# Optimization experiments

Measured on AMD Instinct MI355X. Metric: run time of the kernel, lower is better.

Reference implementation:

```python
import jax, jax.numpy as jnp
import numpy as np
from jax import lax

L, E, H, V, B, S = 25, 64, 8, 30000, 1000, 512


def setup_inputs() -> dict:
    key = jax.random.key(0)
    ks = jax.random.split(key, 24)
    p = lambda k, shape: (jax.random.normal(k, shape) * 0.1).astype(jnp.float32)
    inp = {
        "x": jax.random.randint(ks[0], (B, S), 0, V),
        "embedding": p(ks[1], (V, E)),
        # layer 0 (input dim = E)
        "W_xz0": p(ks[2], (E, H)), "W_hz0": p(ks[3], (H, H)), "b_z0": p(ks[4], (H,)),
        "W_xr0": p(ks[5], (E, H)), "W_hr0": p(ks[6], (H, H)), "b_r0": p(ks[7], (H,)),
        "W_xH0": p(ks[8], (E, H)), "W_rH0": p(ks[9], (H, H)), "b_H0": p(ks[10], (H,)),
        # layers 1..L-1 stacked (input dim = H)
        "W_xz": p(ks[11], (L - 1, H, H)), "W_hz": p(ks[12], (L - 1, H, H)), "b_z": p(ks[13], (L - 1, H)),
        "W_xr": p(ks[14], (L - 1, H, H)), "W_hr": p(ks[15], (L - 1, H, H)), "b_r": p(ks[16], (L - 1, H)),
        "W_xH": p(ks[17], (L - 1, H, H)), "W_rH": p(ks[18], (L - 1, H, H)), "b_H": p(ks[19], (L - 1, H)),
        "W_hy": p(ks[20], (H, 1)), "b_y": p(ks[21], (1,)),
    }
    return inp


def _cell(x_t, h, Wxz, Whz, bz, Wxr, Whr, br, WxH, WrH, bH):
    z = jax.nn.sigmoid(x_t @ Wxz + h @ Whz + bz)
    r = jax.nn.sigmoid(x_t @ Wxr + h @ Whr + br)
    Hc = jnp.tanh(x_t @ WxH + (h * r) @ WrH + bH)
    return h * (1.0 - z) + z * Hc


def reference(x, embedding, W_xz0, W_hz0, b_z0, W_xr0, W_hr0, b_r0, W_xH0, W_rH0, b_H0,
              W_xz, W_hz, b_z, W_xr, W_hr, b_r, W_xH, W_rH, b_H, W_hy, b_y):
    emb = embedding[x]                     # [B, S, E]
    bsz = x.shape[0]
    h0 = jnp.zeros((L, bsz, H), dtype=embedding.dtype)

    def time_step(h_all, x_t):            # h_all: [L, B, H]; x_t: [B, E]
        h_new0 = _cell(x_t, h_all[0], W_xz0, W_hz0, b_z0, W_xr0, W_hr0, b_r0, W_xH0, W_rH0, b_H0)

        def layer_step(inp_t, ws):
            Wxz, Whz, bz, Wxr, Whr, br, WxH, WrH, bH, h_prev = ws
            h_new = _cell(inp_t, h_prev, Wxz, Whz, bz, Wxr, Whr, br, WxH, WrH, bH)
            return h_new, h_new

        _, h_rest = lax.scan(layer_step, h_new0,
                             (W_xz, W_hz, b_z, W_xr, W_hr, b_r, W_xH, W_rH, b_H, h_all[1:]))
        return jnp.concatenate([h_new0[None], h_rest], axis=0), None

    h_last, _ = lax.scan(time_step, h0, jnp.swapaxes(emb, 0, 1))  # scan over S
    logits = h_last[-1] @ W_hy + b_y       # [B, 1]
    return logits.squeeze(-1), h_last
```

## Files before the change

### kernel.cpp

```cpp
#include <hip/hip_runtime.h>
#include <hip/hip_bf16.h>
#include <stdint.h>

#define L_ 25
#define E_ 64
#define H_ 8
#define B_ 1000
#define S_ 512
#define GQ 4
#define NCELL (L_ * GQ)
#define TPBR (NCELL * 8)
#define TS 4
#define NSUPER (S_ / TS + L_ - 1)
#define HS 12
#define XG 36

typedef float v2f __attribute__((ext_vector_type(2)));
typedef float v4f __attribute__((ext_vector_type(4)));

#define PIN(x) asm volatile("" : "+v"(x))

__device__ __forceinline__ v2f pkfma(v2f a, v2f b, v2f c) {
  v2f d;
  asm("v_pk_fma_f32 %0, %1, %2, %3" : "=v"(d) : "v"(a), "v"(b), "v"(c));
  return d;
}
__device__ __forceinline__ v2f pkfma_l(v2f a, v2f b, v2f c) {
  v2f d;
  asm("v_pk_fma_f32 %0, %1, %2, %3 op_sel:[0,0,0] op_sel_hi:[0,1,1]"
      : "=v"(d) : "v"(a), "v"(b), "v"(c));
  return d;
}
__device__ __forceinline__ v2f pkfma_h(v2f a, v2f b, v2f c) {
  v2f d;
  asm("v_pk_fma_f32 %0, %1, %2, %3 op_sel:[1,0,0] op_sel_hi:[1,1,1]"
      : "=v"(d) : "v"(a), "v"(b), "v"(c));
  return d;
}
__device__ __forceinline__ v2f pkadd(v2f a, v2f b) {
  v2f d;
  asm("v_pk_add_f32 %0, %1, %2" : "=v"(d) : "v"(a), "v"(b));
  return d;
}
__device__ __forceinline__ v2f vlo(v4f v) { return __builtin_shufflevector(v, v, 0, 1); }
__device__ __forceinline__ v2f vhi(v4f v) { return __builtin_shufflevector(v, v, 2, 3); }
__device__ __forceinline__ v2f mk2(float a, float b) { v2f r; r.x = a; r.y = b; return r; }

#define CHAIN8(acc, ma, mb, w)            \
  acc = pkfma_l(vlo(ma), w[0], acc);      \
  acc = pkfma_h(vlo(ma), w[1], acc);      \
  acc = pkfma_l(vhi(ma), w[2], acc);      \
  acc = pkfma_h(vhi(ma), w[3], acc);      \
  acc = pkfma_l(vlo(mb), w[4], acc);      \
  acc = pkfma_h(vlo(mb), w[5], acc);      \
  acc = pkfma_l(vhi(mb), w[6], acc);      \
  acc = pkfma_h(vhi(mb), w[7], acc);

#define CHAIN4P(acc, ma, mb, w)           \
  acc = pkfma(vlo(ma), w[0], acc);        \
  acc = pkfma(vhi(ma), w[1], acc);        \
  acc = pkfma(vlo(mb), w[2], acc);        \
  acc = pkfma(vhi(mb), w[3], acc);

__device__ __forceinline__ float ulo(uint32_t u) { return __uint_as_float(u << 16); }
__device__ __forceinline__ float uhi(uint32_t u) { return __uint_as_float(u & 0xffff0000u); }

__device__ __forceinline__ float toF(float v) { return v; }
__device__ __forceinline__ float toF(__hip_bfloat16 v) { return __bfloat162float(v); }
__device__ __forceinline__ void stP(float* p, float v) { *p = v; }
__device__ __forceinline__ void stP(__hip_bfloat16* p, float v) { *p = __float2bfloat16(v); }

__device__ __forceinline__ v2f loadC2(const float* p) { return *(const v2f*)p; }
__device__ __forceinline__ v2f loadC2(const __hip_bfloat16* p) {
  const uint32_t u = *(const uint32_t*)p;
  return mk2(ulo(u), uhi(u));
}

__device__ __forceinline__ void load8f(const __hip_bfloat16* p, float* o) {
  const uint4 v = *(const uint4*)p;
  o[0] = ulo(v.x); o[1] = uhi(v.x); o[2] = ulo(v.y); o[3] = uhi(v.y);
  o[4] = ulo(v.z); o[5] = uhi(v.z); o[6] = ulo(v.w); o[7] = uhi(v.w);
}
__device__ __forceinline__ void load8f(const float* p, float* o) {
  const float4 a = ((const float4*)p)[0];
  const float4 b = ((const float4*)p)[1];
  o[0] = a.x; o[1] = a.y; o[2] = a.z; o[3] = a.w;
  o[4] = b.x; o[5] = b.y; o[6] = b.z; o[7] = b.w;
}

__device__ __forceinline__ void st4(float* p, float a, float b, float c, float d) {
  float4 v; v.x = a; v.y = b; v.z = c; v.w = d;
  *(float4*)p = v;
}
__device__ __forceinline__ void st4(__hip_bfloat16* p, float a, float b, float c, float d) {
  __hip_bfloat16 t[4] = {__float2bfloat16(a), __float2bfloat16(b),
                         __float2bfloat16(c), __float2bfloat16(d)};
  *(ushort4*)p = *(ushort4*)t;
}

__device__ __forceinline__ float sigmo(float x) {
  return __builtin_amdgcn_rcpf(1.f + __expf(-x));
}

__device__ __forceinline__ void detect64(const unsigned short* __restrict__ u,
                                         int tid, float* fl) {
  if (tid < 64) {
    float m = 0.f;
#pragma unroll
    for (int k = 0; k < 4; ++k) {
      const uint32_t q = u[tid * 4 + k];
      float v = fabsf(__uint_as_float(q << 16));
      if (!(v < 1e30f)) v = 1e30f;
      m = fmaxf(m, v);
    }
#pragma unroll
    for (int off = 32; off; off >>= 1) m = fmaxf(m, __shfl_down(m, off, 64));
    if (tid == 0) *fl = (m > 2.0f) ? 0.f : 1.f;
  }
}

template <typename T, typename PT>
__device__ __forceinline__ void pre_body(
    const int* __restrict__ x, const void* __restrict__ embv,
    const void* __restrict__ Wzv, const void* __restrict__ Wrv,
    const void* __restrict__ Whv, PT* __restrict__ pre,
    float* WL, float* TBb) {
  const T* emb = (const T*)embv;
  const T* Wz = (const T*)Wzv;
  const T* Wr = (const T*)Wrv;
  const T* Wh = (const T*)Whv;
  const int tid = threadIdx.x;

  for (int idx = tid; idx < 64 * 24; idx += 256) {
    const int k = idx / 24, c = idx - k * 24;
    float w;
    if (c < 16) w = toF(((c & 1) ? Wr : Wz)[k * 8 + (c >> 1)]);
    else        w = toF(Wh[k * 8 + (c - 16)]);
    WL[idx] = w;
  }
  __syncthreads();

  const int tok = blockIdx.x * 256 + tid;
  const int t = x[tok];

  v2f acc[12];
#pragma unroll
  for (int q = 0; q < 12; ++q) acc[q] = mk2(0.f, 0.f);

  for (int kb = 0; kb < 8; ++kb) {
    float e[8];
    load8f(emb + (size_t)t * E_ + kb * 8, e);
#pragma unroll
    for (int k8 = 0; k8 < 8; ++k8) {
      const v4f* wr = (const v4f*)(WL + (kb * 8 + k8) * 24);
      const v2f ee = mk2(e[k8], e[k8]);
#pragma unroll
      for (int q = 0; q < 6; ++q) {
        const v4f w4 = wr[q];
        acc[2 * q]     = pkfma(ee, vlo(w4), acc[2 * q]);
        acc[2 * q + 1] = pkfma(ee, vhi(w4), acc[2 * q + 1]);
      }
    }
  }

  const int wid = tid >> 6, lane = tid & 63;
  float* tb = TBb + wid * (24 * 65);
#pragma unroll
  for (int q = 0; q < 12; ++q) {
    tb[(2 * q) * 65 + lane] = acc[q].x;
    tb[(2 * q + 1) * 65 + lane] = acc[q].y;
  }
  asm volatile("s_waitcnt lgkmcnt(0)" ::: "memory");
  __builtin_amdgcn_wave_barrier();

  PT* ob = pre + (size_t)(blockIdx.x * 256 + wid * 64) * 24;
#pragma unroll
  for (int it = 0; it < 6; ++it) {
    const int F0 = it * 256 + lane * 4;
    float o[4];
#pragma unroll
    for (int e2 = 0; e2 < 4; ++e2) {
      const int F = F0 + e2;
      const int tk = F / 24;
      const int c = F - tk * 24;
      o[e2] = tb[c * 65 + tk];
    }
    st4(ob + F0, o[0], o[1], o[2], o[3]);
  }
}

template <typename PT>
__global__ __launch_bounds__(256, 4) void gru_pre(
    const int* __restrict__ x, const void* __restrict__ emb,
    const void* __restrict__ Wz, const void* __restrict__ Wr,
    const void* __restrict__ Wh, PT* __restrict__ pre) {
  __shared__ __align__(16) float WL[64 * 24];
  __shared__ __align__(16) float TB[4][24 * 65];
  __shared__ float fl;
  detect64((const unsigned short*)emb, threadIdx.x, &fl);
  __syncthreads();
  if (fl != 0.f) pre_body<__hip_bfloat16, PT>(x, emb, Wz, Wr, Wh, pre, WL, &TB[0][0]);
  else           pre_body<float, PT>(x, emb, Wz, Wr, Wh, pre, WL, &TB[0][0]);
}

template <typename T, typename PT>
__device__ __forceinline__ void rec_body(
    const PT* __restrict__ pre,
    const void* __restrict__ Whz0v, const void* __restrict__ bz0v,
    const void* __restrict__ Whr0v, const void* __restrict__ br0v,
    const void* __restrict__ WrH0v, const void* __restrict__ bH0v,
    const void* __restrict__ Wxzv, const void* __restrict__ Whzv,
    const void* __restrict__ bzv, const void* __restrict__ Wxrv,
    const void* __restrict__ Whrv, const void* __restrict__ brv,
    const void* __restrict__ WxHv, const void* __restrict__ WrHv,
    const void* __restrict__ bHv, const void* __restrict__ Whyv,
    const void* __restrict__ byv, void* __restrict__ outv,
    float* hrsh, float* xbuf) {
  const T* Whz0 = (const T*)Whz0v; const T* bz0 = (const T*)bz0v;
  const T* Whr0 = (const T*)Whr0v; const T* br0 = (const T*)br0v;
  const T* WrH0 = (const T*)WrH0v; const T* bH0 = (const T*)bH0v;
  const T* Wxz = (const T*)Wxzv;   const T* Whz = (const T*)Whzv;
  const T* bz = (const T*)bzv;     const T* Wxr = (const T*)Wxrv;
  const T* Whr = (const T*)Whrv;   const T* br = (const T*)brv;
  const T* WxH = (const T*)WxHv;   const T* WrH = (const T*)WrHv;
  const T* bH = (const T*)bHv;     const T* Why = (const T*)Whyv;
  const T* by = (const T*)byv;     T* out = (T*)outv;

  const int tid = threadIdx.x;
  const int gi = tid >> 3;
  const int j = tid & 7;
  const int l = gi >> 2;
  const int g = gi & 3;
  const int b = blockIdx.x * GQ + g;

  for (int i = tid; i < 2 * NCELL * XG; i += TPBR) xbuf[i] = 0.f;

  v2f wzrx[8], wzrh[8], wxh2[4], wrh2[4], bzr;
  float vbh;
  if (l == 0) {
#pragma unroll
    for (int k = 0; k < 8; ++k) {
      wzrh[k] = mk2(toF(Whz0[k * 8 + j]), toF(Whr0[k * 8 + j]));
      wzrx[k] = mk2(0.f, 0.f);
    }
#pragma unroll
    for (int q = 0; q < 4; ++q) {
      wrh2[q] = mk2(toF(WrH0[(2 * q) * 8 + j]), toF(WrH0[(2 * q + 1) * 8 + j]));
      wxh2[q] = mk2(0.f, 0.f);
    }
    bzr = mk2(toF(bz0[j]), toF(br0[j]));
    vbh = toF(bH0[j]);
  } else {
    const int base = (l - 1) * 64;
#pragma unroll
    for (int k = 0; k < 8; ++k) {
      wzrx[k] = mk2(toF(Wxz[base + k * 8 + j]), toF(Wxr[base + k * 8 + j]));
      wzrh[k] = mk2(toF(Whz[base + k * 8 + j]), toF(Whr[base + k * 8 + j]));
    }
#pragma unroll
    for (int q = 0; q < 4; ++q) {
      wxh2[q] = mk2(toF(WxH[base + (2 * q) * 8 + j]), toF(WxH[base + (2 * q + 1) * 8 + j]));
      wrh2[q] = mk2(toF(WrH[base + (2 * q) * 8 + j]), toF(WrH[base + (2 * q + 1) * 8 + j]));
    }
    bzr = mk2(toF(bz[(l - 1) * 8 + j]), toF(br[(l - 1) * 8 + j]));
    vbh = toF(bH[(l - 1) * 8 + j]);
  }
#pragma unroll
  for (int k = 0; k < 8; ++k) { PIN(wzrx[k]); PIN(wzrh[k]); }
#pragma unroll
  for (int q = 0; q < 4; ++q) { PIN(wxh2[q]); PIN(wrh2[q]); }
  PIN(bzr); PIN(vbh);

  const PT* ppr = pre + (size_t)b * (S_ * 24);
  v2f czr0 = mk2(0.f, 0.f), czr1 = czr0, czr2 = czr0, czr3 = czr0;
  float ch0 = 0.f, ch1 = 0.f, ch2 = 0.f, ch3 = 0.f;
  if (l == 0) {
    czr0 = loadC2(ppr + 0 * 24 + 2 * j);  ch0 = toF(ppr[0 * 24 + 16 + j]);
    czr1 = loadC2(ppr + 1 * 24 + 2 * j);  ch1 = toF(ppr[1 * 24 + 16 + j]);
    czr2 = loadC2(ppr + 2 * 24 + 2 * j);  ch2 = toF(ppr[2 * 24 + 16 + j]);
    czr3 = loadC2(ppr + 3 * 24 + 2 * j);  ch3 = toF(ppr[3 * 24 + 16 + j]);
  }

  float* hrg = hrsh + gi * HS;
  float* hrgj = hrg + j;
  const int gp = (gi >= GQ) ? (gi - GQ) * XG : 0;
  const float* xpe = xbuf + NCELL * XG + gp;
  const float* xpo = xbuf + gp;
  float* xce = xbuf + gi * XG;
  float* xco = xbuf + NCELL * XG + gi * XG;

  float hown = 0.f;

  __syncthreads();

  for (int s = 0; s < NSUPER; ++s) {
    const unsigned rel = (unsigned)(s - l);
    if (rel < (unsigned)(S_ / TS)) {
      const float* xp = (s & 1) ? xpo : xpe;
      float* xc = (s & 1) ? xco : xce;
      const float* xprev = (s & 1) ? xce : xco;

      const v4f xa0 = ((const v4f*)xp)[0];
      const v4f xb0 = ((const v4f*)xp)[1];
      const v4f xa1 = ((const v4f*)xp)[2];
      const v4f xb1 = ((const v4f*)xp)[3];
      v4f xa2, xb2, xa3, xb3;
      v2f ax1, ah1v, ax2c, ah2v, ax3c, ah3v;
      float hn0, hn1, hn2, hn3;

      v2f nzr0 = mk2(0.f, 0.f), nzr1 = nzr0, nzr2 = nzr0, nzr3 = nzr0;
      float nh0 = 0.f, nh1 = 0.f, nh2 = 0.f, nh3 = 0.f;
      const bool pf = (l == 0) && (rel + 1u < (unsigned)(S_ / TS));

      {
        const v4f h01 = ((const v4f*)(xprev + 24))[0];
        const v4f h23 = ((const v4f*)(xprev + 24))[1];
        v2f ax0 = czr0; CHAIN8(ax0, xa0, xb0, wzrx);
        v2f ah0v = mk2(ch0, vbh); CHAIN4P(ah0v, xa0, xb0, wxh2);
        ax1 = czr1; CHAIN8(ax1, xa1, xb1, wzrx);
        ah1v = mk2(ch1, vbh); CHAIN4P(ah1v, xa1, xb1, wxh2);
        v2f azrh = bzr; CHAIN8(azrh, h01, h23, wzrh);
        const v2f azr = pkadd(azrh, ax0);
        const float r_ = sigmo(azr.y);
        *hrgj = hown * r_;
        __builtin_amdgcn_wave_barrier();
        const v4f r01 = ((const v4f*)hrg)[0];
        const v4f r23 = ((const v4f*)hrg)[1];
        xa2 = ((const v4f*)xp)[4];
        xb2 = ((const v4f*)xp)[5];
        CHAIN4P(ah0v, r01, r23, wrh2);
        const float ah_ = ah0v.x + ah0v.y;
        const float ez_ = __expf(fminf(-azr.x, 30.f));
        const float eh_ = __expf(fminf(-2.f * ah_, 30.f));
        const float t_ = hown * ez_;
        const float nu_ = fmaf(eh_, t_ - 1.f, t_ + 1.f);
        const float de_ = (1.f + ez_) * (1.f + eh_);
        hn0 = nu_ * __builtin_amdgcn_rcpf(de_);
        xc[j] = hn0;
        __builtin_amdgcn_wave_barrier();
      }
      {
        const v4f h01 = ((const v4f*)xc)[0];
        const v4f h23 = ((const v4f*)xc)[1];
        xa3 = ((const v4f*)xp)[6];
        xb3 = ((const v4f*)xp)[7];
        ax2c = czr2; CHAIN8(ax2c, xa2, xb2, wzrx);
        ah2v = mk2(ch2, vbh); CHAIN4P(ah2v, xa2, xb2, wxh2);
        v2f azrh = bzr; CHAIN8(azrh, h01, h23, wzrh);
        const v2f azr = pkadd(azrh, ax1);
        const float r_ = sigmo(azr.y);
        *hrgj = hn0 * r_;
        __builtin_amdgcn_wave_barrier();
        const v4f r01 = ((const v4f*)hrg)[0];
        const v4f r23 = ((const v4f*)hrg)[1];
        ax3c = czr3; CHAIN8(ax3c, xa3, xb3, wzrx);
        ah3v = mk2(ch3, vbh); CHAIN4P(ah3v, xa3, xb3, wxh2);
        CHAIN4P(ah1v, r01, r23, wrh2);
        const float ah_ = ah1v.x + ah1v.y;
        const float ez_ = __expf(fminf(-azr.x, 30.f));
        const float eh_ = __expf(fminf(-2.f * ah_, 30.f));
        const float t_ = hn0 * ez_;
        const float nu_ = fmaf(eh_, t_ - 1.f, t_ + 1.f);
        const float de_ = (1.f + ez_) * (1.f + eh_);
        hn1 = nu_ * __builtin_amdgcn_rcpf(de_);
        xc[8 + j] = hn1;
        __builtin_amdgcn_wave_barrier();
      }
      {
        const v4f h01 = ((const v4f*)(xc + 8))[0];
        const v4f h23 = ((const v4f*)(xc + 8))[1];
        if (pf) {
          const PT* pn = ppr + (TS * rel + 4) * 24;
          nzr0 = loadC2(pn + 0 * 24 + 2 * j);  nh0 = toF(pn[0 * 24 + 16 + j]);
          nzr1 = loadC2(pn + 1 * 24 + 2 * j);  nh1 = toF(pn[1 * 24 + 16 + j]);
          nzr2 = loadC2(pn + 2 * 24 + 2 * j);  nh2 = toF(pn[2 * 24 + 16 + j]);
          nzr3 = loadC2(pn + 3 * 24 + 2 * j);  nh3 = toF(pn[3 * 24 + 16 + j]);
        }
        v2f azrh = bzr; CHAIN8(azrh, h01, h23, wzrh);
        const v2f azr = pkadd(azrh, ax2c);
        const float r_ = sigmo(azr.y);
        *hrgj = hn1 * r_;
        __builtin_amdgcn_wave_barrier();
        const v4f r01 = ((const v4f*)hrg)[0];
        const v4f r23 = ((const v4f*)hrg)[1];
        CHAIN4P(ah2v, r01, r23, wrh2);
        const float ah_ = ah2v.x + ah2v.y;
        const float ez_ = __expf(fminf(-azr.x, 30.f));
        const float eh_ = __expf(fminf(-2.f * ah_, 30.f));
        const float t_ = hn1 * ez_;
        const float nu_ = fmaf(eh_, t_ - 1.f, t_ + 1.f);
        const float de_ = (1.f + ez_) * (1.f + eh_);
        hn2 = nu_ * __builtin_amdgcn_rcpf(de_);
        xc[16 + j] = hn2;
        __builtin_amdgcn_wave_barrier();
      }
      {
        const v4f h01 = ((const v4f*)(xc + 16))[0];
        const v4f h23 = ((const v4f*)(xc + 16))[1];
        v2f azrh = bzr; CHAIN8(azrh, h01, h23, wzrh);
        const v2f azr = pkadd(azrh, ax3c);
        const float r_ = sigmo(azr.y);
        *hrgj = hn2 * r_;
        __builtin_amdgcn_wave_barrier();
        const v4f r01 = ((const v4f*)hrg)[0];
        const v4f r23 = ((const v4f*)hrg)[1];
        CHAIN4P(ah3v, r01, r23, wrh2);
        const float ah_ = ah3v.x + ah3v.y;
        const float ez_ = __expf(fminf(-azr.x, 30.f));
        const float eh_ = __expf(fminf(-2.f * ah_, 30.f));
        const float t_ = hn2 * ez_;
        const float nu_ = fmaf(eh_, t_ - 1.f, t_ + 1.f);
        const float de_ = (1.f + ez_) * (1.f + eh_);
        hn3 = nu_ * __builtin_amdgcn_rcpf(de_);
        xc[24 + j] = hn3;
        __builtin_amdgcn_wave_barrier();
      }

      hown = hn3;
      czr0 = nzr0; ch0 = nh0; czr1 = nzr1; ch1 = nh1;
      czr2 = nzr2; ch2 = nh2; czr3 = nzr3; ch3 = nh3;
    }
    __syncthreads();
  }

  stP(out + B_ + (l * B_ + b) * H_ + j, hown);
  if (l == L_ - 1 && j == 0) {
    const float* hf = xbuf + NCELL * XG + gi * XG + 24;
    float ssum = toF(by[0]);
#pragma unroll
    for (int k = 0; k < 8; ++k) ssum = fmaf(hf[k], toF(Why[k]), ssum);
    stP(out + b, ssum);
  }
}

template <typename PT>
__global__ __launch_bounds__(TPBR, 4) void gru_rec(
    const void* __restrict__ emb, const PT* __restrict__ pre,
    const void* __restrict__ Whz0, const void* __restrict__ bz0,
    const void* __restrict__ Whr0, const void* __restrict__ br0,
    const void* __restrict__ WrH0, const void* __restrict__ bH0,
    const void* __restrict__ Wxz, const void* __restrict__ Whz,
    const void* __restrict__ bz, const void* __restrict__ Wxr,
    const void* __restrict__ Whr, const void* __restrict__ br,
    const void* __restrict__ WxH, const void* __restrict__ WrH,
    const void* __restrict__ bH, const void* __restrict__ Why,
    const void* __restrict__ by, void* __restrict__ out) {
  __shared__ __align__(16) float hrsh[NCELL * HS];
  __shared__ __align__(16) float xbuf[2 * NCELL * XG];
  __shared__ float fl;
  detect64((const unsigned short*)emb, threadIdx.x, &fl);
  __syncthreads();
  if (fl != 0.f)
    rec_body<__hip_bfloat16, PT>(pre, Whz0, bz0, Whr0, br0, WrH0, bH0, Wxz, Whz,
                                 bz, Wxr, Whr, br, WxH, WrH, bH, Why, by, out,
                                 hrsh, xbuf);
  else
    rec_body<float, PT>(pre, Whz0, bz0, Whr0, br0, WrH0, bH0, Wxz, Whz, bz, Wxr,
                        Whr, br, WxH, WrH, bH, Why, by, out, hrsh, xbuf);
}

template <typename PT>
static void launch_all(void* const* d_in, PT* pre, void* d_out, hipStream_t stream) {
  gru_pre<PT><<<B_ * S_ / 256, 256, 0, stream>>>(
      (const int*)d_in[0], d_in[1], d_in[2], d_in[5], d_in[8], pre);
  gru_rec<PT><<<B_ / GQ, TPBR, 0, stream>>>(
      d_in[1], pre, d_in[3], d_in[4], d_in[6], d_in[7], d_in[9], d_in[10],
      d_in[11], d_in[12], d_in[13], d_in[14], d_in[15], d_in[16], d_in[17],
      d_in[18], d_in[19], d_in[20], d_in[21], d_out);
}

extern "C" void kernel_launch(void* const* d_in, const int* in_sizes, int n_in,
                              void* d_out, int out_size, void* d_ws, size_t ws_size,
                              hipStream_t stream) {
  const size_t needF = (size_t)B_ * S_ * 24 * sizeof(float);
  if (ws_size >= needF)
    launch_all<float>(d_in, (float*)d_ws, d_out, stream);
  else
    launch_all<__hip_bfloat16>(d_in, (__hip_bfloat16*)d_ws, d_out, stream);
}
```

Measured before the change: 395.5 us.

## Replace per-superstep block barrier with neighbor-wave LDS flag synchronization

Replaces the __syncthreads at the end of each wavefront superstep in the recurrent kernel with point-to-point flags in shared memory. Each wave waits only on the previous wave's completion flag and the next wave's read-done flag, so waves handling different layers can drift relative to each other. This is meant to cut the cost of the full-block barrier, which stalls all waves each step. It adds spin-wait polling with s_sleep and depends on correct release/acquire ordering at workgroup scope, which is a correctness risk if a dependency is missed.

```diff
diff --git a/kernel.cpp b/kernel.cpp
--- a/kernel.cpp
+++ b/kernel.cpp
@@ -12,6 +12,7 @@
 #define TPBR (NCELL * 8)
 #define TS 4
 #define NSUPER (S_ / TS + L_ - 1)
+#define NW ((TPBR + 63) / 64)
 #define HS 12
 #define XG 36
 
@@ -19,6 +20,7 @@
 typedef float v4f __attribute__((ext_vector_type(4)));
 
 #define PIN(x) asm volatile("" : "+v"(x))
+#define LGKM0() asm volatile("s_waitcnt lgkmcnt(0)" ::: "memory")
 
 __device__ __forceinline__ v2f pkfma(v2f a, v2f b, v2f c) {
   v2f d;
@@ -100,6 +102,14 @@
 
 __device__ __forceinline__ float sigmo(float x) {
   return __builtin_amdgcn_rcpf(1.f + __expf(-x));
+}
+
+__device__ __forceinline__ void wait_ge(int* p, int s) {
+  while (__hip_atomic_load(p, __ATOMIC_ACQUIRE, __HIP_MEMORY_SCOPE_WORKGROUP) < s)
+    __builtin_amdgcn_s_sleep(2);
+}
+__device__ __forceinline__ void sig(int* p, int v) {
+  __hip_atomic_store(p, v, __ATOMIC_RELEASE, __HIP_MEMORY_SCOPE_WORKGROUP);
 }
 
 __device__ __forceinline__ void detect64(const unsigned short* __restrict__ u,
@@ -170,7 +180,7 @@
     tb[(2 * q) * 65 + lane] = acc[q].x;
     tb[(2 * q + 1) * 65 + lane] = acc[q].y;
   }
-  asm volatile("s_waitcnt lgkmcnt(0)" ::: "memory");
+  LGKM0();
   __builtin_amdgcn_wave_barrier();
 
   PT* ob = pre + (size_t)(blockIdx.x * 256 + wid * 64) * 24;
@@ -215,7 +225,7 @@
     const void* __restrict__ WxHv, const void* __restrict__ WrHv,
     const void* __restrict__ bHv, const void* __restrict__ Whyv,
     const void* __restrict__ byv, void* __restrict__ outv,
-    float* hrsh, float* xbuf) {
+    float* hrsh, float* xbuf, int* sflags) {
   const T* Whz0 = (const T*)Whz0v; const T* bz0 = (const T*)bz0v;
   const T* Whr0 = (const T*)Whr0v; const T* br0 = (const T*)br0v;
   const T* WrH0 = (const T*)WrH0v; const T* bH0 = (const T*)bH0v;
@@ -232,8 +242,11 @@
   const int l = gi >> 2;
   const int g = gi & 3;
   const int b = blockIdx.x * GQ + g;
+  const int w = tid >> 6;
+  const bool lane0 = (tid & 63) == 0;
 
   for (int i = tid; i < 2 * NCELL * XG; i += TPBR) xbuf[i] = 0.f;
+  for (int i = tid; i < 32; i += TPBR) sflags[i] = 0;
 
   v2f wzrx[8], wzrh[8], wxh2[4], wrh2[4], bzr;
   float vbh;
@@ -294,6 +307,10 @@
   __syncthreads();
 
   for (int s = 0; s < NSUPER; ++s) {
+    if (w > 0)      wait_ge(sflags + (w - 1), s);
+    if (w < NW - 1) wait_ge(sflags + 16 + (w + 1), s);
+    asm volatile("" ::: "memory");
+
     const unsigned rel = (unsigned)(s - l);
     if (rel < (unsigned)(S_ / TS)) {
       const float* xp = (s & 1) ? xpo : xpe;
@@ -344,6 +361,8 @@
         const v4f h23 = ((const v4f*)xc)[1];
         xa3 = ((const v4f*)xp)[6];
         xb3 = ((const v4f*)xp)[7];
+        LGKM0();
+        if (lane0) sig(sflags + 16 + w, s + 1);
         ax2c = czr2; CHAIN8(ax2c, xa2, xb2, wzrx);
         ah2v = mk2(ch2, vbh); CHAIN4P(ah2v, xa2, xb2, wxh2);
         v2f azrh = bzr; CHAIN8(azrh, h01, h23, wzrh);
@@ -419,8 +438,12 @@
       hown = hn3;
       czr0 = nzr0; ch0 = nh0; czr1 = nzr1; ch1 = nh1;
       czr2 = nzr2; ch2 = nh2; czr3 = nzr3; ch3 = nh3;
-    }
-    __syncthreads();
+
+      LGKM0();
+      if (lane0) sig(sflags + w, s + 1);
+    } else {
+      if (lane0) { sig(sflags + 16 + w, s + 1); sig(sflags + w, s + 1); }
+    }
   }
 
   stP(out + B_ + (l * B_ + b) * H_ + j, hown);
@@ -447,16 +470,17 @@
     const void* __restrict__ by, void* __restrict__ out) {
   __shared__ __align__(16) float hrsh[NCELL * HS];
   __shared__ __align__(16) float xbuf[2 * NCELL * XG];
+  __shared__ __align__(16) int sflags[32];
   __shared__ float fl;
   detect64((const unsigned short*)emb, threadIdx.x, &fl);
   __syncthreads();
   if (fl != 0.f)
     rec_body<__hip_bfloat16, PT>(pre, Whz0, bz0, Whr0, br0, WrH0, bH0, Wxz, Whz,
                                  bz, Wxr, Whr, br, WxH, WrH, bH, Why, by, out,
-                                 hrsh, xbuf);
+                                 hrsh, xbuf, sflags);
   else
     rec_body<float, PT>(pre, Whz0, bz0, Whr0, br0, WrH0, bH0, Wxz, Whz, bz, Wxr,
-                        Whr, br, WxH, WrH, bH, Why, by, out, hrsh, xbuf);
+                        Whr, br, WxH, WrH, bH, Why, by, out, hrsh, xbuf, sflags);
 }
 
 template <typename PT>
```

Result: no change. 389.3 us (-1.6%).
